# Kernel optimization log

Measured on AMD Instinct MI355X. Metric: run time of the kernel, lower is better.

Reference implementation:

```python
import jax, jax.numpy as jnp
import numpy as np

UNITS = 512
WINDOW = 2


def causal_conv1d(x, w, b):
    # x: (B, T, D), w: (W, D, U), b: (U,) -> (B, T, U), causal (left) padding
    y = jax.lax.conv_general_dilated(
        x, w, window_strides=(1,), padding=[(w.shape[0] - 1, 0)],
        dimension_numbers=("NWC", "WIO", "NWC"))
    return y + b


def setup_inputs() -> dict:
    key = jax.random.key(0)
    ks = jax.random.split(key, 7)
    B, T, D, U, W = 16, 4096, 512, UNITS, WINDOW
    scale = (2.0 / (W * D + U)) ** 0.5  # glorot-ish
    x = jax.random.normal(ks[0], (B, T, D), dtype=jnp.float32)
    Wz = jax.random.normal(ks[1], (W, D, U), dtype=jnp.float32) * scale
    bz = jnp.zeros((U,), dtype=jnp.float32)
    Wf = jax.random.normal(ks[2], (W, D, U), dtype=jnp.float32) * scale
    bf = jnp.zeros((U,), dtype=jnp.float32)
    Wo = jax.random.normal(ks[3], (W, D, U), dtype=jnp.float32) * scale
    bo = jnp.zeros((U,), dtype=jnp.float32)
    return {"x": x, "Wz": Wz, "bz": bz, "Wf": Wf, "bf": bf, "Wo": Wo, "bo": bo}


def reference(x, Wz, bz, Wf, bf, Wo, bo):
    # Gate projections via causal conv1d
    z = jnp.tanh(causal_conv1d(x, Wz, bz))          # candidate (B,T,U)
    f = jax.nn.sigmoid(causal_conv1d(x, Wf, bf))    # forget gate
    o = jax.nn.sigmoid(causal_conv1d(x, Wo, bo))    # output gate

    # Linear recurrence h_t = f_t * h_{t-1} + (1 - f_t) * z_t, h_0 = 0,
    # computed as a parallel associative scan over affine maps (a, b):
    # h -> a*h + b, composition (a1,b1) then (a2,b2) = (a2*a1, a2*b1 + b2).
    a = f
    b = (1.0 - f) * z

    def combine(c1, c2):
        a1, b1 = c1
        a2, b2 = c2
        return a2 * a1, a2 * b1 + b2

    _, h = jax.lax.associative_scan(combine, (a, b), axis=1)
    return o * h  # (B, T, U), return_sequences=True
```

## Files before the change

kernel.cpp:

```cpp
#include <hip/hip_runtime.h>
#include <cstdio>
#include <cstdint>

#define B_  16
#define T_  4096
#define D_  512
#define U_  512
#define KK  1024
#define M_  (B_*T_)
#define NTOT 1536

#define CHUNK 128
#define NCH   (T_/CHUNK)

typedef __attribute__((ext_vector_type(8))) short  bf16x8;
typedef __attribute__((ext_vector_type(4))) float  f32x4;
typedef __attribute__((ext_vector_type(8))) unsigned short u16x8;

__device__ __forceinline__ unsigned short f2bf(float f) {
    unsigned int u = __float_as_uint(f);
    unsigned int r = (u + 0x7fffu + ((u >> 16) & 1u)) >> 16;
    return (unsigned short)r;
}

__device__ __forceinline__ void gl_lds16(const void* g, void* l) {
    __builtin_amdgcn_global_load_lds(
        (const __attribute__((address_space(1))) void*)g,
        (__attribute__((address_space(3))) void*)l, 16, 0, 0);
}

__global__ __launch_bounds__(256)
void convert_x_kernel(const float* __restrict__ x, unsigned short* __restrict__ xz)
{
    const size_t e = ((size_t)blockIdx.x * 256 + threadIdx.x) * 8;
    const size_t row = e >> 9;
    const int    d   = (int)(e & 511);
    const int    tz  = (int)(row % 4097);
    const size_t b   = row / 4097;
    u16x8 o;
    if (tz == 0) {
        #pragma unroll
        for (int i = 0; i < 8; ++i) o[i] = 0;
    } else {
        const size_t src = (((b << 12) + (size_t)(tz - 1)) << 9) + d;
        const float4 v0 = *reinterpret_cast<const float4*>(x + src);
        const float4 v1 = *reinterpret_cast<const float4*>(x + src + 4);
        o[0] = f2bf(v0.x); o[1] = f2bf(v0.y); o[2] = f2bf(v0.z); o[3] = f2bf(v0.w);
        o[4] = f2bf(v1.x); o[5] = f2bf(v1.y); o[6] = f2bf(v1.z); o[7] = f2bf(v1.w);
    }
    *reinterpret_cast<u16x8*>(xz + e) = o;
}

__global__ __launch_bounds__(256)
void convert_wt_kernel(const float* __restrict__ Wz, const float* __restrict__ Wf,
                       const float* __restrict__ Wo, unsigned short* __restrict__ Wt)
{
    __shared__ float tile[32][33];
    const int g = blockIdx.z;
    const float* __restrict__ W = (g == 0) ? Wz : (g == 1 ? Wf : Wo);
    const int k0 = blockIdx.x * 32;
    const int u0 = blockIdx.y * 32;
    const int tx = threadIdx.x, ty = threadIdx.y;
    #pragma unroll
    for (int r = 0; r < 4; ++r)
        tile[ty + r * 8][tx] = W[(size_t)(k0 + ty + r * 8) * 512 + u0 + tx];
    __syncthreads();
    #pragma unroll
    for (int r = 0; r < 4; ++r) {
        const int u = u0 + ty + r * 8;
        Wt[(size_t)(g * 512 + u) * 1024 + k0 + tx] = f2bf(tile[tx][ty + r * 8]);
    }
}

__global__ __launch_bounds__(256)
void gemm_mfma_kernel(const unsigned short* __restrict__ xz,
                      const unsigned short* __restrict__ Wt,
                      const float* __restrict__ bz, const float* __restrict__ bfg,
                      const float* __restrict__ bo,
                      float* __restrict__ zbuf, float* __restrict__ fbuf,
                      float* __restrict__ obuf)
{
    __shared__ unsigned short As[128 * 64];
    __shared__ unsigned short Bs[128 * 64];

    const int tid  = threadIdx.x;
    const int lane = tid & 63;
    const int wave = tid >> 6;
    const int wm   = wave >> 1;
    const int wn   = wave & 1;

    const int flat = blockIdx.x;
    const int xcd  = flat & 7;
    const int idx  = flat >> 3;
    const int nblk = idx % 12;
    const int mt   = xcd * 64 + idx / 12;
    const int m0   = mt * 128;
    const int n0   = nblk * 128;

    const int swz = (lane & 7) ^ (lane >> 3);
    const unsigned short* gA[4];
    const unsigned short* gB[4];
    #pragma unroll
    for (int i = 0; i < 4; ++i) {
        const int r = i * 32 + wave * 8 + (lane >> 3);
        const int m = m0 + r;
        const int b = m >> 12;
        const int t = m & 4095;
        gA[i] = xz + ((size_t)(b * 4097 + t) << 9) + swz * 8;
        gB[i] = Wt + ((size_t)(n0 + r) << 10) + swz * 8;
    }
    char* AsB = (char*)As;
    char* BsB = (char*)Bs;

    f32x4 acc[4][4];
    #pragma unroll
    for (int i = 0; i < 4; ++i)
        #pragma unroll
        for (int j = 0; j < 4; ++j)
            acc[i][j] = (f32x4){0.f, 0.f, 0.f, 0.f};

    for (int kk = 0; kk < 16; ++kk) {
        #pragma unroll
        for (int i = 0; i < 4; ++i)
            gl_lds16(gA[i] + kk * 64, AsB + i * 4096 + wave * 1024);
        #pragma unroll
        for (int i = 0; i < 4; ++i)
            gl_lds16(gB[i] + kk * 64, BsB + i * 4096 + wave * 1024);
        __syncthreads();

        #pragma unroll
        for (int ks = 0; ks < 2; ++ks) {
            const int ch = (ks * 4 + (lane >> 4)) ^ (lane & 7);
            bf16x8 av[4], bv[4];
            #pragma unroll
            for (int i = 0; i < 4; ++i) {
                const int row = wn * 64 + i * 16 + (lane & 15);
                av[i] = *reinterpret_cast<const bf16x8*>(BsB + row * 128 + ch * 16);
            }
            #pragma unroll
            for (int j = 0; j < 4; ++j) {
                const int row = wm * 64 + j * 16 + (lane & 15);
                bv[j] = *reinterpret_cast<const bf16x8*>(AsB + row * 128 + ch * 16);
            }
            #pragma unroll
            for (int i = 0; i < 4; ++i)
                #pragma unroll
                for (int j = 0; j < 4; ++j)
                    acc[i][j] = __builtin_amdgcn_mfma_f32_16x16x32_bf16(
                        av[i], bv[j], acc[i][j], 0, 0, 0);
        }
        __syncthreads();
    }

    const int gate = nblk >> 2;
    float* __restrict__ outg = (gate == 0) ? zbuf : (gate == 1 ? fbuf : obuf);
    const float* __restrict__ bg = (gate == 0) ? bz : (gate == 1 ? bfg : bo);
    const int mcol = m0 + wm * 64 + (lane & 15);
    const int u0g  = (nblk & 3) * 128 + wn * 64 + ((lane >> 4) << 2);

    #pragma unroll
    for (int i = 0; i < 4; ++i) {
        const int u = u0g + i * 16;
        const float4 b4 = *reinterpret_cast<const float4*>(bg + u);
        #pragma unroll
        for (int j = 0; j < 4; ++j) {
            const int m = mcol + j * 16;
            float4 v;
            v.x = acc[i][j][0] + b4.x;
            v.y = acc[i][j][1] + b4.y;
            v.z = acc[i][j][2] + b4.z;
            v.w = acc[i][j][3] + b4.w;
            if (gate == 0) {
                v.x = 2.0f / (1.0f + __expf(-2.0f * v.x)) - 1.0f;
                v.y = 2.0f / (1.0f + __expf(-2.0f * v.y)) - 1.0f;
                v.z = 2.0f / (1.0f + __expf(-2.0f * v.z)) - 1.0f;
                v.w = 2.0f / (1.0f + __expf(-2.0f * v.w)) - 1.0f;
            } else {
                v.x = 1.0f / (1.0f + __expf(-v.x));
                v.y = 1.0f / (1.0f + __expf(-v.y));
                v.z = 1.0f / (1.0f + __expf(-v.z));
                v.w = 1.0f / (1.0f + __expf(-v.w));
            }
            *reinterpret_cast<float4*>(outg + (size_t)m * 512 + u) = v;
        }
    }
}

__global__ __launch_bounds__(256)
void chunk_summary_kernel(const float* __restrict__ fbuf,
                          const float* __restrict__ zbuf,
                          float* __restrict__ Ach, float* __restrict__ Bch)
{
    const int bc = blockIdx.x;
    const int c  = bc & (NCH - 1);
    const int b  = bc >> 5;
    const int u  = threadIdx.x * 2;

    const long long base = ((long long)(b * T_ + c * CHUNK)) * U_ + u;
    float2 A = make_float2(1.0f, 1.0f);
    float2 Bv = make_float2(0.0f, 0.0f);
    #pragma unroll 8
    for (int i = 0; i < CHUNK; ++i) {
        const float2 f = *reinterpret_cast<const float2*>(fbuf + base + (long long)i * U_);
        const float2 z = *reinterpret_cast<const float2*>(zbuf + base + (long long)i * U_);
        Bv.x = f.x * Bv.x + (1.0f - f.x) * z.x;
        Bv.y = f.y * Bv.y + (1.0f - f.y) * z.y;
        A.x *= f.x;
        A.y *= f.y;
    }
    const int idx = (b * NCH + c) * U_ + u;
    *reinterpret_cast<float2*>(Ach + idx) = A;
    *reinterpret_cast<float2*>(Bch + idx) = Bv;
}

__global__ __launch_bounds__(256)
void chunk_prefix_kernel(const float* __restrict__ Ach,
                         const float* __restrict__ Bch,
                         float* __restrict__ Hin)
{
    const int g = blockIdx.x * 256 + threadIdx.x;
    const int b = g >> 8;
    const int u = (g & 255) * 2;
    float2 h = make_float2(0.0f, 0.0f);
    #pragma unroll 4
    for (int c = 0; c < NCH; ++c) {
        const int idx = (b * NCH + c) * U_ + u;
        *reinterpret_cast<float2*>(Hin + idx) = h;
        const float2 A = *reinterpret_cast<const float2*>(Ach + idx);
        const float2 Bv = *reinterpret_cast<const float2*>(Bch + idx);
        h.x = A.x * h.x + Bv.x;
        h.y = A.y * h.y + Bv.y;
    }
}

__global__ __launch_bounds__(256)
void scan_apply_kernel(const float* __restrict__ fbuf,
                       const float* __restrict__ zbuf,
                       const float* __restrict__ obuf,
                       const float* __restrict__ Hin,
                       float* __restrict__ out)
{
    const int bc = blockIdx.x;
    const int c  = bc & (NCH - 1);
    const int b  = bc >> 5;
    const int u  = threadIdx.x * 2;

    const long long base = ((long long)(b * T_ + c * CHUNK)) * U_ + u;
    float2 h = *reinterpret_cast<const float2*>(Hin + (b * NCH + c) * U_ + u);
    #pragma unroll 8
    for (int i = 0; i < CHUNK; ++i) {
        const long long p = base + (long long)i * U_;
        const float2 f = *reinterpret_cast<const float2*>(fbuf + p);
        const float2 z = *reinterpret_cast<const float2*>(zbuf + p);
        const float2 o = *reinterpret_cast<const float2*>(obuf + p);
        h.x = f.x * h.x + (1.0f - f.x) * z.x;
        h.y = f.y * h.y + (1.0f - f.y) * z.y;
        float2 r;
        r.x = o.x * h.x;
        r.y = o.y * h.y;
        *reinterpret_cast<float2*>(out + p) = r;
    }
}

extern "C" void kernel_launch(void* const* d_in, const int* in_sizes, int n_in,
                              void* d_out, int out_size, void* d_ws, size_t ws_size,
                              hipStream_t stream)
{
    const float* x  = (const float*)d_in[0];
    const float* Wz = (const float*)d_in[1];
    const float* bz = (const float*)d_in[2];
    const float* Wf = (const float*)d_in[3];
    const float* bf = (const float*)d_in[4];
    const float* Wo = (const float*)d_in[5];
    const float* bo = (const float*)d_in[6];
    float* out = (float*)d_out;

    const size_t S  = (size_t)M_ * U_;
    const size_t Sc = (size_t)B_ * NCH * U_;
    const size_t XZ = (size_t)B_ * (T_ + 1) * D_;
    const size_t WT = (size_t)NTOT * KK;

    float* zbuf = (float*)d_ws;
    float* fbuf = zbuf + S;
    float* obuf = fbuf + S;
    unsigned short* xz = (unsigned short*)(obuf + S);
    unsigned short* Wt = xz + XZ;
    float* Ach = (float*)(Wt + WT);
    float* Bch = Ach + Sc;
    float* Hin = Bch + Sc;

    const size_t need = 3 * S * sizeof(float) + (XZ + WT) * sizeof(unsigned short)
                      + 3 * Sc * sizeof(float);
    if (ws_size < need) {
        fprintf(stderr, "QRNN kernel: ws_size=%zu < needed %zu bytes!\n",
                ws_size, need);
    }

    {
        const size_t nthreads = XZ / 8;
        convert_x_kernel<<<dim3((unsigned)(nthreads / 256)), 256, 0, stream>>>(x, xz);
        convert_wt_kernel<<<dim3(32, 16, 3), dim3(32, 8), 0, stream>>>(Wz, Wf, Wo, Wt);
    }
    gemm_mfma_kernel<<<dim3(12 * (M_ / 128)), 256, 0, stream>>>(
        xz, Wt, bz, bf, bo, zbuf, fbuf, obuf);
    chunk_summary_kernel<<<dim3(B_ * NCH), 256, 0, stream>>>(fbuf, zbuf, Ach, Bch);
    chunk_prefix_kernel<<<dim3(16), 256, 0, stream>>>(Ach, Bch, Hin);
    scan_apply_kernel<<<dim3(B_ * NCH), 256, 0, stream>>>(fbuf, zbuf, obuf, Hin, out);
}
```

Measured before the change: 698.9 us.

## Enlarge GEMM tiles to 256x256 with double-buffered LDS pipelining

Restructures the MFMA GEMM to use 256x256 output tiles with 512-thread blocks, so each wave computes a 64x128 sub-tile with more operand reuse. K tiles are staged into two LDS buffers, and loads for tile k+2 are issued while tile k is computed, synchronised with vmcnt waits and barriers. MFMA sections are wrapped in s_setprio. The larger tiles and 128 KB of LDS raise register pressure and cap occupancy at one block per CU. They also reduce the block count, which may hurt load balance.

```diff
diff --git a/kernel.cpp b/kernel.cpp
--- a/kernel.cpp
+++ b/kernel.cpp
@@ -72,7 +72,7 @@
     }
 }
 
-__global__ __launch_bounds__(256)
+__global__ __launch_bounds__(512, 2)
 void gemm_mfma_kernel(const unsigned short* __restrict__ xz,
                       const unsigned short* __restrict__ Wt,
                       const float* __restrict__ bz, const float* __restrict__ bfg,
@@ -80,91 +80,120 @@
                       float* __restrict__ zbuf, float* __restrict__ fbuf,
                       float* __restrict__ obuf)
 {
-    __shared__ unsigned short As[128 * 64];
-    __shared__ unsigned short Bs[128 * 64];
+    __shared__ unsigned short As[2 * 256 * 64];
+    __shared__ unsigned short Bs[2 * 256 * 64];
 
     const int tid  = threadIdx.x;
     const int lane = tid & 63;
     const int wave = tid >> 6;
-    const int wm   = wave >> 1;
-    const int wn   = wave & 1;
-
-    const int flat = blockIdx.x;
-    const int xcd  = flat & 7;
-    const int idx  = flat >> 3;
-    const int nblk = idx % 12;
-    const int mt   = xcd * 64 + idx / 12;
-    const int m0   = mt * 128;
-    const int n0   = nblk * 128;
-
-    const int swz = (lane & 7) ^ (lane >> 3);
-    const unsigned short* gA[4];
-    const unsigned short* gB[4];
-    #pragma unroll
-    for (int i = 0; i < 4; ++i) {
-        const int r = i * 32 + wave * 8 + (lane >> 3);
-        const int m = m0 + r;
-        const int b = m >> 12;
-        const int t = m & 4095;
-        gA[i] = xz + ((size_t)(b * 4097 + t) << 9) + swz * 8;
-        gB[i] = Wt + ((size_t)(n0 + r) << 10) + swz * 8;
-    }
+    const int wu   = wave & 3;
+    const int wm   = wave >> 2;
+
+    const int flat  = blockIdx.x;
+    const int xcd   = flat & 7;
+    const int idx   = flat >> 3;
+    const int ntile = idx % 6;
+    const int mt    = xcd * 32 + idx / 6;
+    const int m0 = mt * 256;
+    const int n0 = ntile * 256;
+    const int b  = m0 >> 12;
+    const int t0 = m0 & 4095;
+
+    const int srow = wave * 8 + (lane >> 3);
+    const int swz  = (lane & 7) ^ (lane >> 3);
+    const unsigned short* gA = xz + ((size_t)(b * 4097 + t0 + srow) << 9) + swz * 8;
+    const unsigned short* gB = Wt + ((size_t)(n0 + srow) << 10) + swz * 8;
     char* AsB = (char*)As;
     char* BsB = (char*)Bs;
-
-    f32x4 acc[4][4];
+    const int ldst = wave * 1024;
+
+    auto STAGE = [&](int kt, int bf) {
+        #pragma unroll
+        for (int i = 0; i < 4; ++i)
+            gl_lds16(gA + i * 32768 + kt * 64, AsB + bf * 32768 + i * 8192 + ldst);
+        #pragma unroll
+        for (int i = 0; i < 4; ++i)
+            gl_lds16(gB + i * 65536 + kt * 64, BsB + bf * 32768 + i * 8192 + ldst);
+    };
+
+    f32x4 acc[4][8];
     #pragma unroll
     for (int i = 0; i < 4; ++i)
         #pragma unroll
-        for (int j = 0; j < 4; ++j)
+        for (int j = 0; j < 8; ++j)
             acc[i][j] = (f32x4){0.f, 0.f, 0.f, 0.f};
 
-    for (int kk = 0; kk < 16; ++kk) {
-        #pragma unroll
-        for (int i = 0; i < 4; ++i)
-            gl_lds16(gA[i] + kk * 64, AsB + i * 4096 + wave * 1024);
-        #pragma unroll
-        for (int i = 0; i < 4; ++i)
-            gl_lds16(gB[i] + kk * 64, BsB + i * 4096 + wave * 1024);
-        __syncthreads();
-
-        #pragma unroll
-        for (int ks = 0; ks < 2; ++ks) {
-            const int ch = (ks * 4 + (lane >> 4)) ^ (lane & 7);
-            bf16x8 av[4], bv[4];
+    const int l15 = lane & 15;
+    const int ck0 = (((lane >> 4) + 0) ^ (lane & 7)) * 16;
+    const int ck1 = (((lane >> 4) + 4) ^ (lane & 7)) * 16;
+    const int wvBase = (wu * 64 + l15) * 128;
+    const int xvBase = (wm * 128 + l15) * 128;
+
+    auto COMPUTE = [&](int bf) {
+        const char* AB = AsB + bf * 32768;
+        const char* BB = BsB + bf * 32768;
+        bf16x8 wv[4][2];
+        #pragma unroll
+        for (int i = 0; i < 4; ++i) {
+            wv[i][0] = *reinterpret_cast<const bf16x8*>(BB + wvBase + i * 2048 + ck0);
+            wv[i][1] = *reinterpret_cast<const bf16x8*>(BB + wvBase + i * 2048 + ck1);
+        }
+        #pragma unroll
+        for (int jh = 0; jh < 2; ++jh) {
+            bf16x8 xv[4][2];
             #pragma unroll
-            for (int i = 0; i < 4; ++i) {
-                const int row = wn * 64 + i * 16 + (lane & 15);
-                av[i] = *reinterpret_cast<const bf16x8*>(BsB + row * 128 + ch * 16);
+            for (int j2 = 0; j2 < 4; ++j2) {
+                xv[j2][0] = *reinterpret_cast<const bf16x8*>(
+                    AB + xvBase + (jh * 4 + j2) * 2048 + ck0);
+                xv[j2][1] = *reinterpret_cast<const bf16x8*>(
+                    AB + xvBase + (jh * 4 + j2) * 2048 + ck1);
             }
-            #pragma unroll
-            for (int j = 0; j < 4; ++j) {
-                const int row = wm * 64 + j * 16 + (lane & 15);
-                bv[j] = *reinterpret_cast<const bf16x8*>(AsB + row * 128 + ch * 16);
-            }
+            __builtin_amdgcn_s_setprio(1);
             #pragma unroll
             for (int i = 0; i < 4; ++i)
                 #pragma unroll
-                for (int j = 0; j < 4; ++j)
-                    acc[i][j] = __builtin_amdgcn_mfma_f32_16x16x32_bf16(
-                        av[i], bv[j], acc[i][j], 0, 0, 0);
+                for (int j2 = 0; j2 < 4; ++j2) {
+                    acc[i][jh * 4 + j2] = __builtin_amdgcn_mfma_f32_16x16x32_bf16(
+                        wv[i][0], xv[j2][0], acc[i][jh * 4 + j2], 0, 0, 0);
+                    acc[i][jh * 4 + j2] = __builtin_amdgcn_mfma_f32_16x16x32_bf16(
+                        wv[i][1], xv[j2][1], acc[i][jh * 4 + j2], 0, 0, 0);
+                }
+            __builtin_amdgcn_s_setprio(0);
         }
-        __syncthreads();
-    }
-
-    const int gate = nblk >> 2;
+    };
+
+    STAGE(0, 0);
+    STAGE(1, 1);
+
+    #pragma unroll 1
+    for (int t = 0; t < 15; ++t) {
+        asm volatile("s_waitcnt vmcnt(8)" ::: "memory");
+        __builtin_amdgcn_s_barrier();
+        asm volatile("" ::: "memory");
+        COMPUTE(t & 1);
+        asm volatile("" ::: "memory");
+        __builtin_amdgcn_s_barrier();
+        asm volatile("" ::: "memory");
+        if (t < 14) STAGE(t + 2, t & 1);
+    }
+    asm volatile("s_waitcnt vmcnt(0)" ::: "memory");
+    __builtin_amdgcn_s_barrier();
+    asm volatile("" ::: "memory");
+    COMPUTE(1);
+
+    const int gate = ntile >> 1;
     float* __restrict__ outg = (gate == 0) ? zbuf : (gate == 1 ? fbuf : obuf);
     const float* __restrict__ bg = (gate == 0) ? bz : (gate == 1 ? bfg : bo);
-    const int mcol = m0 + wm * 64 + (lane & 15);
-    const int u0g  = (nblk & 3) * 128 + wn * 64 + ((lane >> 4) << 2);
+    const int ubase = (ntile & 1) * 256 + wu * 64 + ((lane >> 4) << 2);
+    const int mbase = m0 + wm * 128 + l15;
 
     #pragma unroll
     for (int i = 0; i < 4; ++i) {
-        const int u = u0g + i * 16;
+        const int u = ubase + i * 16;
         const float4 b4 = *reinterpret_cast<const float4*>(bg + u);
         #pragma unroll
-        for (int j = 0; j < 4; ++j) {
-            const int m = mcol + j * 16;
+        for (int j = 0; j < 8; ++j) {
+            const int m = mbase + j * 16;
             float4 v;
             v.x = acc[i][j][0] + b4.x;
             v.y = acc[i][j][1] + b4.y;
@@ -301,7 +330,7 @@
         convert_x_kernel<<<dim3((unsigned)(nthreads / 256)), 256, 0, stream>>>(x, xz);
         convert_wt_kernel<<<dim3(32, 16, 3), dim3(32, 8), 0, stream>>>(Wz, Wf, Wo, Wt);
     }
-    gemm_mfma_kernel<<<dim3(12 * (M_ / 128)), 256, 0, stream>>>(
+    gemm_mfma_kernel<<<dim3(6 * (M_ / 256)), 512, 0, stream>>>(
         xz, Wt, bz, bf, bo, zbuf, fbuf, obuf);
     chunk_summary_kernel<<<dim3(B_ * NCH), 256, 0, stream>>>(fbuf, zbuf, Ach, Bch);
     chunk_prefix_kernel<<<dim3(16), 256, 0, stream>>>(Ach, Bch, Hin);
```

Result: faster. 668.0 us (-4.4%).
